# Optimization experiments

Hardware: AMD Instinct MI355X
Metric: run time of the kernel (lower is better)

## Reference

```python
import jax, jax.numpy as jnp
import numpy as np

B, S, E, H = 2, 2048, 1024, 16
D = E // H  # head_dim = 64


def setup_inputs() -> dict:
    key = jax.random.key(0)
    ks = jax.random.split(key, 5)
    return {
        "hidden_states": jax.random.normal(ks[0], (B, S, E), jnp.float32),
        "c_attn_w": jax.random.normal(ks[1], (E, 3 * E), jnp.float32) * 0.02,
        "c_attn_b": jnp.zeros((3 * E,), jnp.float32),
        "c_proj_w": jax.random.normal(ks[2], (E, E), jnp.float32) * 0.02,
        "c_proj_b": jnp.zeros((E,), jnp.float32),
    }


def reference(hidden_states, c_attn_w, c_attn_b, c_proj_w, c_proj_b):
    # Conv1D: x @ w + b -> qkv [B, S, 3E]
    qkv = hidden_states @ c_attn_w + c_attn_b
    q, k, v = jnp.split(qkv, 3, axis=-1)
    # [B, H, S, D]
    q = q.reshape(B, S, H, D).transpose(0, 2, 1, 3)
    k = k.reshape(B, S, H, D).transpose(0, 2, 1, 3)
    v = v.reshape(B, S, H, D).transpose(0, 2, 1, 3)
    # scores [B, H, S, S], scaled by sqrt(head_dim)
    scores = jnp.einsum("bhqd,bhkd->bhqk", q, k) / jnp.sqrt(jnp.asarray(D, q.dtype))
    causal = jnp.tril(jnp.ones((S, S), bool))  # [S, S]
    mask_value = jnp.finfo(scores.dtype).min
    scores = jnp.where(causal, scores, mask_value)
    attn = jax.nn.softmax(scores, axis=-1)
    # attn @ V -> [B, H, S, D] -> [B, S, E]
    out = jnp.einsum("bhqk,bhkd->bhqd", attn, v)
    out = out.transpose(0, 2, 1, 3).reshape(B, S, E)
    return out @ c_proj_w + c_proj_b
```

## Files before the change

kernel.cpp:

```cpp
#include <hip/hip_runtime.h>

using bf16 = __bf16;
typedef __bf16 bf16x8 __attribute__((ext_vector_type(8)));
typedef __bf16 bf16x4 __attribute__((ext_vector_type(4)));
typedef float  f32x4  __attribute__((ext_vector_type(4)));

#define MFMA16(a, b, c) __builtin_amdgcn_mfma_f32_16x16x32_bf16((a), (b), (c), 0, 0, 0)

static constexpr int S = 2048, E = 1024;
static constexpr float CSCALE = 0.18033688011112042f;

__device__ __forceinline__ void gld16(const bf16* g, bf16* l) {
    __builtin_amdgcn_global_load_lds((const __attribute__((address_space(1))) unsigned*)g,
                                     (__attribute__((address_space(3))) unsigned*)l, 16, 0, 0);
}

__global__ __launch_bounds__(256) void k_prep(const float* __restrict__ hs, const float* __restrict__ w0,
                                              const float* __restrict__ w1, bf16* __restrict__ A0,
                                              bf16* __restrict__ Wt0, bf16* __restrict__ Wt1) {
    __shared__ float tile[32][33];
    const int bx = blockIdx.x;
    if (bx < 4096) {
        int i = (bx * 256 + threadIdx.x) * 4;
        float4 v = *(const float4*)(hs + i);
        bf16x4 o = { (bf16)v.x, (bf16)v.y, (bf16)v.z, (bf16)v.w };
        *(bf16x4*)(A0 + i) = o;
        return;
    }
    const float* in;
    bf16* outp;
    int K, N, nb, kb;
    if (bx < 4096 + 3072) {
        int j = bx - 4096; in = w0; outp = Wt0; K = 1024; N = 3072; nb = j % 96; kb = j / 96;
    } else {
        int j = bx - 7168; in = w1; outp = Wt1; K = 1024; N = 1024; nb = j % 32; kb = j / 32;
    }
    const int bxx = nb * 32, byy = kb * 32;
    const int tx = threadIdx.x & 31, ty = threadIdx.x >> 5;
#pragma unroll
    for (int i = 0; i < 32; i += 8)
        tile[ty + i][tx] = in[(long)(byy + ty + i) * N + bxx + tx];
    __syncthreads();
#pragma unroll
    for (int i = 0; i < 32; i += 8)
        outp[(long)(bxx + ty + i) * K + byy + tx] = (bf16)tile[tx][ty + i];
}

__global__ __launch_bounds__(256) void k_gemm_qkv(const bf16* __restrict__ A, const bf16* __restrict__ Bt,
                                                  const float* __restrict__ bias, bf16* __restrict__ Qs,
                                                  bf16* __restrict__ Kf, bf16* __restrict__ Vf, int Kk) {
    const int bm = blockIdx.x * 128;
    const int bn = blockIdx.y * 128;
    const int tid = threadIdx.x;
    const int w = tid >> 6, lane = tid & 63;
    const int wm = (w >> 1) * 64, wn = (w & 1) * 64;
    const int col = lane & 15, quad = lane >> 4;

    __shared__ __align__(16) char smem[32768];
    bf16* sA = (bf16*)smem;
    bf16* sB = (bf16*)(smem + 16384);
    bf16* T  = (bf16*)smem;

    const bf16* pA[4]; const bf16* pB[4]; bf16* lA[4]; bf16* lB[4];
#pragma unroll
    for (int i = 0; i < 4; i++) {
        const int c = i * 256 + w * 64 + lane;
        const int r = c >> 3, sl = (c & 7) ^ (r & 7);
        pA[i] = A  + (long)(bm + r) * Kk + sl * 8;
        pB[i] = Bt + (long)(bn + r) * Kk + sl * 8;
        lA[i] = sA + i * 2048 + w * 512;
        lB[i] = sB + i * 2048 + w * 512;
    }

    f32x4 acc[4][4] = {};

    for (int k0 = 0; k0 < Kk; k0 += 64) {
        __syncthreads();
#pragma unroll
        for (int i = 0; i < 4; i++) gld16(pA[i] + k0, lA[i]);
#pragma unroll
        for (int i = 0; i < 4; i++) gld16(pB[i] + k0, lB[i]);
        __syncthreads();
#pragma unroll
        for (int h = 0; h < 2; h++) {
            bf16x8 af[4], bfr[4];
#pragma unroll
            for (int mt = 0; mt < 4; mt++) {
                const int row = wm + mt * 16 + col;
                af[mt] = *(const bf16x8*)(sA + row * 64 + (((h * 4 + quad) ^ (col & 7)) * 8));
            }
#pragma unroll
            for (int nt = 0; nt < 4; nt++) {
                const int row = wn + nt * 16 + col;
                bfr[nt] = *(const bf16x8*)(sB + row * 64 + (((h * 4 + quad) ^ (col & 7)) * 8));
            }
#pragma unroll
            for (int mt = 0; mt < 4; mt++)
#pragma unroll
                for (int nt = 0; nt < 4; nt++)
                    acc[mt][nt] = MFMA16(af[mt], bfr[nt], acc[mt][nt]);
        }
    }

    const int seg = bn >> 10;
    const int b = bm >> 11;
    const int kt0 = (bm & 2047) >> 6;

    if (seg == 0) {
#pragma unroll
        for (int mt = 0; mt < 4; mt++) {
            const int gr = bm + wm + mt * 16 + quad * 4;
#pragma unroll
            for (int nt = 0; nt < 4; nt++) {
                const int gc = bn + wn + nt * 16 + col;
                const float bv = bias[gc];
#pragma unroll
                for (int r = 0; r < 4; r++)
                    Qs[(long)(gr + r) * 1024 + gc] = (bf16)((acc[mt][nt][r] + bv) * CSCALE);
            }
        }
        return;
    }

    const int hl = w >> 1;
    if (seg == 1) {
        const int bh = b * 16 + (bn >> 6) - 16 + hl;
#pragma unroll 1
        for (int p = 0; p < 2; p++) {
            __syncthreads();
            if ((wm >> 6) == p) {
#pragma unroll
                for (int mt = 0; mt < 4; mt++) {
                    const int sl = mt * 16 + quad * 4;
#pragma unroll
                    for (int nt = 0; nt < 4; nt++) {
                        const int gcl = wn + nt * 16 + col;
                        const float bv = bias[bn + gcl];
#pragma unroll
                        for (int r = 0; r < 4; r++)
                            T[(sl + r) * 136 + gcl] = (bf16)(acc[mt][nt][r] + bv);
                    }
                }
            }
            __syncthreads();
            const int ktp = kt0 + p;
#pragma unroll
            for (int mi = 0; mi < 2; mi++) {
                const int mt = (w & 1) * 2 + mi;
#pragma unroll
                for (int half = 0; half < 2; half++) {
                    bf16x8 ch = *(const bf16x8*)(T + (mt * 16 + col) * 136 + hl * 64 + half * 32 + quad * 8);
                    const long chunk = ((long)(bh * 32 + ktp) * 8 + mt * 2 + half) * 64 + lane;
                    *(bf16x8*)(Kf + chunk * 8) = ch;
                }
            }
        }
    } else {
        const int bh = b * 16 + (bn >> 6) - 32 + hl;
#pragma unroll 1
        for (int p = 0; p < 2; p++) {
            __syncthreads();
            if ((wm >> 6) == p) {
#pragma unroll
                for (int mt = 0; mt < 4; mt++) {
                    const int sl = mt * 16 + quad * 4;
#pragma unroll
                    for (int nt = 0; nt < 4; nt++) {
                        const int gcl = wn + nt * 16 + col;
                        const float bv = bias[bn + gcl];
                        bf16x4 pk = { (bf16)(acc[mt][nt][0] + bv), (bf16)(acc[mt][nt][1] + bv),
                                      (bf16)(acc[mt][nt][2] + bv), (bf16)(acc[mt][nt][3] + bv) };
                        *(bf16x4*)(T + gcl * 72 + sl) = pk;
                    }
                }
            }
            __syncthreads();
            const int ktp = kt0 + p;
#pragma unroll
            for (int di = 0; di < 2; di++) {
                const int dt = (w & 1) * 2 + di;
#pragma unroll
                for (int ks = 0; ks < 2; ks++) {
                    bf16x8 ch = *(const bf16x8*)(T + (hl * 64 + dt * 16 + col) * 72 + ks * 32 + quad * 8);
                    const long chunk = ((long)(bh * 32 + ktp) * 8 + dt * 2 + ks) * 64 + lane;
                    *(bf16x8*)(Vf + chunk * 8) = ch;
                }
            }
        }
    }
}

__global__ __launch_bounds__(256) void k_gemm_bt64(const bf16* __restrict__ A, const bf16* __restrict__ Bt,
                                                    const float* __restrict__ bias, float* __restrict__ Cout,
                                                    int Mm, int Nn, int Kk) {
    const int bm = blockIdx.x * 64;
    const int bn = blockIdx.y * 128;
    const int tid = threadIdx.x;
    const int w = tid >> 6, lane = tid & 63;
    const int wm = (w >> 1) * 32, wn = (w & 1) * 64;
    const int col = lane & 15, quad = lane >> 4;

    __shared__ bf16 sA[64 * 64];
    __shared__ bf16 sB[128 * 64];

    const bf16* pA[2]; bf16* lA[2];
#pragma unroll
    for (int i = 0; i < 2; i++) {
        const int c = i * 256 + w * 64 + lane;
        const int r = c >> 3, sl = (c & 7) ^ (r & 7);
        pA[i] = A + (long)(bm + r) * Kk + sl * 8;
        lA[i] = sA + i * 2048 + w * 512;
    }
    const bf16* pB[4]; bf16* lB[4];
#pragma unroll
    for (int i = 0; i < 4; i++) {
        const int c = i * 256 + w * 64 + lane;
        const int r = c >> 3, sl = (c & 7) ^ (r & 7);
        pB[i] = Bt + (long)(bn + r) * Kk + sl * 8;
        lB[i] = sB + i * 2048 + w * 512;
    }

    f32x4 acc[2][4] = {};

    for (int k0 = 0; k0 < Kk; k0 += 64) {
        __syncthreads();
#pragma unroll
        for (int i = 0; i < 2; i++) gld16(pA[i] + k0, lA[i]);
#pragma unroll
        for (int i = 0; i < 4; i++) gld16(pB[i] + k0, lB[i]);
        __syncthreads();
#pragma unroll
        for (int h = 0; h < 2; h++) {
            bf16x8 af[2], bfr[4];
#pragma unroll
            for (int mt = 0; mt < 2; mt++) {
                const int row = wm + mt * 16 + col;
                af[mt] = *(const bf16x8*)(sA + row * 64 + (((h * 4 + quad) ^ (col & 7)) * 8));
            }
#pragma unroll
            for (int nt = 0; nt < 4; nt++) {
                const int row = wn + nt * 16 + col;
                bfr[nt] = *(const bf16x8*)(sB + row * 64 + (((h * 4 + quad) ^ (col & 7)) * 8));
            }
#pragma unroll
            for (int mt = 0; mt < 2; mt++)
#pragma unroll
                for (int nt = 0; nt < 4; nt++)
                    acc[mt][nt] = MFMA16(af[mt], bfr[nt], acc[mt][nt]);
        }
    }

#pragma unroll
    for (int mt = 0; mt < 2; mt++) {
        const int gr = bm + wm + mt * 16 + quad * 4;
#pragma unroll
        for (int nt = 0; nt < 4; nt++) {
            const int gc = bn + wn + nt * 16 + col;
            const float bv = bias[gc];
#pragma unroll
            for (int r = 0; r < 4; r++)
                Cout[(long)(gr + r) * Nn + gc] = acc[mt][nt][r] + bv;
        }
    }
}

__global__ __launch_bounds__(128) void k_attn(const bf16* __restrict__ Qs, const bf16* __restrict__ Kf,
                                              const bf16* __restrict__ Vf, bf16* __restrict__ out) {
    const int bh = blockIdx.x & 31;
    const int tp = blockIdx.x >> 5;
    const int b = bh >> 4, h = bh & 15;
    const int tid = threadIdx.x;
    const int w = tid >> 6, lane = tid & 63;
    const int col = lane & 15, quad = lane >> 4;

    __shared__ bf16 sP[2][32 * 72];
    __shared__ float M[2][64][36];
    bf16* pw = sP[w];

    const bf16* kfb = Kf + ((long)bh << 17) + lane * 8;
    const bf16* vfb = Vf + ((long)bh << 17) + lane * 8;

#pragma unroll 1
    for (int sel = 0; sel < 2; sel++) {
        const int t = sel ? 63 - tp : tp;
        const int q0 = t * 32;
        const int nkt = (t >> 1) + 1;
        const int kA = nkt >> 1;
        const int kbeg = w ? kA : 0;
        const int kend = w ? nkt : kA;

        bf16x8 bq[2][2];
#pragma unroll
        for (int qg = 0; qg < 2; qg++) {
            const bf16* qp = Qs + (long)(b * S + q0 + qg * 16 + col) * E + h * 64 + quad * 8;
            bq[qg][0] = *(const bf16x8*)(qp);
            bq[qg][1] = *(const bf16x8*)(qp + 32);
        }
        float m_[2] = { -1e30f, -1e30f }, l_[2] = { 0.f, 0.f };
        f32x4 o[2][4] = {};

#pragma unroll 1
        for (int kt = kbeg; kt < kend; kt++) {
            bf16x8 kfr[4][2], vfr[4][2];
#pragma unroll
            for (int mt = 0; mt < 4; mt++)
#pragma unroll
                for (int half = 0; half < 2; half++)
                    kfr[mt][half] = *(const bf16x8*)(kfb + ((long)(kt * 8 + mt * 2 + half) << 9));
#pragma unroll
            for (int dt = 0; dt < 4; dt++)
#pragma unroll
                for (int ks = 0; ks < 2; ks++)
                    vfr[dt][ks] = *(const bf16x8*)(vfb + ((long)(kt * 8 + dt * 2 + ks) << 9));

            f32x4 s[2][4];
#pragma unroll
            for (int mt = 0; mt < 4; mt++)
#pragma unroll
                for (int qg = 0; qg < 2; qg++) {
                    f32x4 z = {};
                    z = MFMA16(kfr[mt][0], bq[qg][0], z);
                    z = MFMA16(kfr[mt][1], bq[qg][1], z);
                    s[qg][mt] = z;
                }
            if (kt == nkt - 1) {
#pragma unroll
                for (int qg = 0; qg < 2; qg++) {
                    const int qrow = q0 + qg * 16 + col;
#pragma unroll
                    for (int mt = 0; mt < 4; mt++)
#pragma unroll
                        for (int r = 0; r < 4; r++)
                            if (kt * 64 + mt * 16 + quad * 4 + r > qrow) s[qg][mt][r] = -1e30f;
                }
            }
#pragma unroll
            for (int qg = 0; qg < 2; qg++) {
                float cm = -1e30f;
#pragma unroll
                for (int mt = 0; mt < 4; mt++)
#pragma unroll
                    for (int r = 0; r < 4; r++) cm = fmaxf(cm, s[qg][mt][r]);
                cm = fmaxf(cm, __shfl_xor(cm, 16));
                cm = fmaxf(cm, __shfl_xor(cm, 32));
                const float mnew = fmaxf(m_[qg], cm);
                const float alpha = __builtin_amdgcn_exp2f(m_[qg] - mnew);
                m_[qg] = mnew;
                float rs = 0.f;
#pragma unroll
                for (int mt = 0; mt < 4; mt++)
#pragma unroll
                    for (int r = 0; r < 4; r++) {
                        float pe = __builtin_amdgcn_exp2f(s[qg][mt][r] - mnew);
                        s[qg][mt][r] = pe;
                        rs += pe;
                    }
                l_[qg] = l_[qg] * alpha + rs;
#pragma unroll
                for (int dt = 0; dt < 4; dt++)
#pragma unroll
                    for (int r = 0; r < 4; r++) o[qg][dt][r] *= alpha;
#pragma unroll
                for (int mt = 0; mt < 4; mt++) {
                    bf16x4 pk = { (bf16)s[qg][mt][0], (bf16)s[qg][mt][1],
                                  (bf16)s[qg][mt][2], (bf16)s[qg][mt][3] };
                    *(bf16x4*)(pw + (qg * 16 + col) * 72 + mt * 16 + quad * 4) = pk;
                }
            }
#pragma unroll
            for (int ks = 0; ks < 2; ks++) {
                bf16x8 ap[2];
#pragma unroll
                for (int qg = 0; qg < 2; qg++)
                    ap[qg] = *(const bf16x8*)(pw + (qg * 16 + col) * 72 + ks * 32 + quad * 8);
#pragma unroll
                for (int dt = 0; dt < 4; dt++)
#pragma unroll
                    for (int qg = 0; qg < 2; qg++)
                        o[qg][dt] = MFMA16(vfr[dt][ks], ap[qg], o[qg][dt]);
            }
        }

#pragma unroll
        for (int qg = 0; qg < 2; qg++) {
            float lt = l_[qg];
            lt += __shfl_xor(lt, 16);
            lt += __shfl_xor(lt, 32);
            l_[qg] = lt;
        }

        if (w == 0) {
#pragma unroll
            for (int qg = 0; qg < 2; qg++) {
#pragma unroll
                for (int dt = 0; dt < 4; dt++)
                    *(f32x4*)&M[sel][lane][qg * 16 + dt * 4] = o[qg][dt];
                M[sel][lane][32 + qg * 2] = m_[qg];
                M[sel][lane][33 + qg * 2] = l_[qg];
            }
        }
        __syncthreads();
        if (w == 1) {
#pragma unroll
            for (int qg = 0; qg < 2; qg++) {
                const float m0 = M[sel][lane][32 + qg * 2];
                const float l0 = M[sel][lane][33 + qg * 2];
                const float mm = fmaxf(m0, m_[qg]);
                const float a0 = __builtin_amdgcn_exp2f(m0 - mm);
                const float a1 = __builtin_amdgcn_exp2f(m_[qg] - mm);
                const float li = 1.f / (l0 * a0 + l_[qg] * a1);
                bf16* op = out + (long)(b * S + q0 + qg * 16 + col) * E + h * 64 + quad * 4;
#pragma unroll
                for (int dt = 0; dt < 4; dt++) {
                    f32x4 o0 = *(const f32x4*)&M[sel][lane][qg * 16 + dt * 4];
                    bf16x4 ov;
#pragma unroll
                    for (int r = 0; r < 4; r++)
                        ov[r] = (bf16)((o0[r] * a0 + o[qg][dt][r] * a1) * li);
                    *(bf16x4*)(op + dt * 16) = ov;
                }
            }
        }
    }
}

extern "C" void kernel_launch(void* const* d_in, const int* in_sizes, int n_in,
                              void* d_out, int out_size, void* d_ws, size_t ws_size,
                              hipStream_t stream) {
    const float* hs = (const float*)d_in[0];
    const float* w0 = (const float*)d_in[1];
    const float* b0 = (const float*)d_in[2];
    const float* w1 = (const float*)d_in[3];
    const float* b1 = (const float*)d_in[4];
    float* outp = (float*)d_out;

    char* ws = (char*)d_ws;
    bf16* A0    = (bf16*)(ws);
    bf16* Wt0   = (bf16*)(ws + 8388608);
    bf16* Wt1   = (bf16*)(ws + 14680064);
    bf16* Qs    = (bf16*)(ws + 16777216);
    bf16* Kf    = (bf16*)(ws + 25165824);
    bf16* Vf    = (bf16*)(ws + 33554432);
    bf16* attnO = (bf16*)(ws + 41943040);

    k_prep<<<8192, 256, 0, stream>>>(hs, w0, w1, A0, Wt0, Wt1);
    k_gemm_qkv<<<dim3(32, 24), 256, 0, stream>>>(A0, Wt0, b0, Qs, Kf, Vf, 1024);
    k_attn<<<1024, 128, 0, stream>>>(Qs, Kf, Vf, attnO);
    k_gemm_bt64<<<dim3(64, 8), 256, 0, stream>>>(attnO, Wt1, b1, outp, 4096, 1024, 1024);
}
```

Measured before the change: 178.5 us.

## Split attention blocks to one query tile each and widen weight transpose tiles

The attention kernel used to pair a short and a long causal query tile in each block and loop over both. It now gives each block a single query tile, doubles the grid, and launches the longest tiles first so the scheduler can balance the load. The weight-transpose prep kernel now handles 64x32 tiles per block, which halves the number of transpose blocks and widens each bf16 store row. The trade-off is more, smaller attention blocks, so Q loads and block launch overhead are no longer amortized across a tile pair.

```diff
diff --git a/kernel.cpp b/kernel.cpp
--- a/kernel.cpp
+++ b/kernel.cpp
@@ -18,7 +18,7 @@
 __global__ __launch_bounds__(256) void k_prep(const float* __restrict__ hs, const float* __restrict__ w0,
                                               const float* __restrict__ w1, bf16* __restrict__ A0,
                                               bf16* __restrict__ Wt0, bf16* __restrict__ Wt1) {
-    __shared__ float tile[32][33];
+    __shared__ float tile[64][33];
     const int bx = blockIdx.x;
     if (bx < 4096) {
         int i = (bx * 256 + threadIdx.x) * 4;
@@ -30,20 +30,25 @@
     const float* in;
     bf16* outp;
     int K, N, nb, kb;
-    if (bx < 4096 + 3072) {
-        int j = bx - 4096; in = w0; outp = Wt0; K = 1024; N = 3072; nb = j % 96; kb = j / 96;
-    } else {
-        int j = bx - 7168; in = w1; outp = Wt1; K = 1024; N = 1024; nb = j % 32; kb = j / 32;
-    }
-    const int bxx = nb * 32, byy = kb * 32;
-    const int tx = threadIdx.x & 31, ty = threadIdx.x >> 5;
-#pragma unroll
-    for (int i = 0; i < 32; i += 8)
-        tile[ty + i][tx] = in[(long)(byy + ty + i) * N + bxx + tx];
+    const int j = bx - 4096;
+    if (j < 1536) { in = w0; outp = Wt0; K = 1024; N = 3072; nb = j % 96; kb = j / 96; }
+    else          { in = w1; outp = Wt1; K = 1024; N = 1024; nb = (j - 1536) % 32; kb = (j - 1536) / 32; }
+    const int bxx = nb * 32, byy = kb * 64;
+    {
+        const int r0 = threadIdx.x >> 5, c = threadIdx.x & 31;
+#pragma unroll
+        for (int i = 0; i < 8; i++)
+            tile[r0 + i * 8][c] = in[(long)(byy + r0 + i * 8) * N + bxx + c];
+    }
     __syncthreads();
-#pragma unroll
-    for (int i = 0; i < 32; i += 8)
-        outp[(long)(bxx + ty + i) * K + byy + tx] = (bf16)tile[tx][ty + i];
+    {
+        const int n0 = threadIdx.x >> 6, k = threadIdx.x & 63;
+#pragma unroll
+        for (int i = 0; i < 8; i++) {
+            const int n = n0 + i * 4;
+            outp[(long)(bxx + n) * K + byy + k] = (bf16)tile[k][n];
+        }
+    }
 }
 
 __global__ __launch_bounds__(256) void k_gemm_qkv(const bf16* __restrict__ A, const bf16* __restrict__ Bt,
@@ -267,158 +272,153 @@
 __global__ __launch_bounds__(128) void k_attn(const bf16* __restrict__ Qs, const bf16* __restrict__ Kf,
                                               const bf16* __restrict__ Vf, bf16* __restrict__ out) {
     const int bh = blockIdx.x & 31;
-    const int tp = blockIdx.x >> 5;
+    const int t = 63 - (blockIdx.x >> 5);
     const int b = bh >> 4, h = bh & 15;
     const int tid = threadIdx.x;
     const int w = tid >> 6, lane = tid & 63;
     const int col = lane & 15, quad = lane >> 4;
+    const int q0 = t * 32;
+    const int nkt = (t >> 1) + 1;
+    const int kA = nkt >> 1;
+    const int kbeg = w ? kA : 0;
+    const int kend = w ? nkt : kA;
 
     __shared__ bf16 sP[2][32 * 72];
-    __shared__ float M[2][64][36];
+    __shared__ float M[64][36];
     bf16* pw = sP[w];
 
     const bf16* kfb = Kf + ((long)bh << 17) + lane * 8;
     const bf16* vfb = Vf + ((long)bh << 17) + lane * 8;
 
+    bf16x8 bq[2][2];
+#pragma unroll
+    for (int qg = 0; qg < 2; qg++) {
+        const bf16* qp = Qs + (long)(b * S + q0 + qg * 16 + col) * E + h * 64 + quad * 8;
+        bq[qg][0] = *(const bf16x8*)(qp);
+        bq[qg][1] = *(const bf16x8*)(qp + 32);
+    }
+    float m_[2] = { -1e30f, -1e30f }, l_[2] = { 0.f, 0.f };
+    f32x4 o[2][4] = {};
+
 #pragma unroll 1
-    for (int sel = 0; sel < 2; sel++) {
-        const int t = sel ? 63 - tp : tp;
-        const int q0 = t * 32;
-        const int nkt = (t >> 1) + 1;
-        const int kA = nkt >> 1;
-        const int kbeg = w ? kA : 0;
-        const int kend = w ? nkt : kA;
-
-        bf16x8 bq[2][2];
+    for (int kt = kbeg; kt < kend; kt++) {
+        bf16x8 kfr[4][2], vfr[4][2];
+#pragma unroll
+        for (int mt = 0; mt < 4; mt++)
+#pragma unroll
+            for (int half = 0; half < 2; half++)
+                kfr[mt][half] = *(const bf16x8*)(kfb + ((long)(kt * 8 + mt * 2 + half) << 9));
+#pragma unroll
+        for (int dt = 0; dt < 4; dt++)
+#pragma unroll
+            for (int ks = 0; ks < 2; ks++)
+                vfr[dt][ks] = *(const bf16x8*)(vfb + ((long)(kt * 8 + dt * 2 + ks) << 9));
+
+        f32x4 s[2][4];
+#pragma unroll
+        for (int mt = 0; mt < 4; mt++)
+#pragma unroll
+            for (int qg = 0; qg < 2; qg++) {
+                f32x4 z = {};
+                z = MFMA16(kfr[mt][0], bq[qg][0], z);
+                z = MFMA16(kfr[mt][1], bq[qg][1], z);
+                s[qg][mt] = z;
+            }
+        if (kt == nkt - 1) {
+#pragma unroll
+            for (int qg = 0; qg < 2; qg++) {
+                const int qrow = q0 + qg * 16 + col;
+#pragma unroll
+                for (int mt = 0; mt < 4; mt++)
+#pragma unroll
+                    for (int r = 0; r < 4; r++)
+                        if (kt * 64 + mt * 16 + quad * 4 + r > qrow) s[qg][mt][r] = -1e30f;
+            }
+        }
 #pragma unroll
         for (int qg = 0; qg < 2; qg++) {
-            const bf16* qp = Qs + (long)(b * S + q0 + qg * 16 + col) * E + h * 64 + quad * 8;
-            bq[qg][0] = *(const bf16x8*)(qp);
-            bq[qg][1] = *(const bf16x8*)(qp + 32);
-        }
-        float m_[2] = { -1e30f, -1e30f }, l_[2] = { 0.f, 0.f };
-        f32x4 o[2][4] = {};
-
-#pragma unroll 1
-        for (int kt = kbeg; kt < kend; kt++) {
-            bf16x8 kfr[4][2], vfr[4][2];
+            float cm = -1e30f;
 #pragma unroll
             for (int mt = 0; mt < 4; mt++)
 #pragma unroll
-                for (int half = 0; half < 2; half++)
-                    kfr[mt][half] = *(const bf16x8*)(kfb + ((long)(kt * 8 + mt * 2 + half) << 9));
+                for (int r = 0; r < 4; r++) cm = fmaxf(cm, s[qg][mt][r]);
+            cm = fmaxf(cm, __shfl_xor(cm, 16));
+            cm = fmaxf(cm, __shfl_xor(cm, 32));
+            const float mnew = fmaxf(m_[qg], cm);
+            const float alpha = __builtin_amdgcn_exp2f(m_[qg] - mnew);
+            m_[qg] = mnew;
+            float rs = 0.f;
+#pragma unroll
+            for (int mt = 0; mt < 4; mt++)
+#pragma unroll
+                for (int r = 0; r < 4; r++) {
+                    float pe = __builtin_amdgcn_exp2f(s[qg][mt][r] - mnew);
+                    s[qg][mt][r] = pe;
+                    rs += pe;
+                }
+            l_[qg] = l_[qg] * alpha + rs;
 #pragma unroll
             for (int dt = 0; dt < 4; dt++)
 #pragma unroll
-                for (int ks = 0; ks < 2; ks++)
-                    vfr[dt][ks] = *(const bf16x8*)(vfb + ((long)(kt * 8 + dt * 2 + ks) << 9));
-
-            f32x4 s[2][4];
-#pragma unroll
-            for (int mt = 0; mt < 4; mt++)
-#pragma unroll
-                for (int qg = 0; qg < 2; qg++) {
-                    f32x4 z = {};
-                    z = MFMA16(kfr[mt][0], bq[qg][0], z);
-                    z = MFMA16(kfr[mt][1], bq[qg][1], z);
-                    s[qg][mt] = z;
-                }
-            if (kt == nkt - 1) {
-#pragma unroll
-                for (int qg = 0; qg < 2; qg++) {
-                    const int qrow = q0 + qg * 16 + col;
-#pragma unroll
-                    for (int mt = 0; mt < 4; mt++)
-#pragma unroll
-                        for (int r = 0; r < 4; r++)
-                            if (kt * 64 + mt * 16 + quad * 4 + r > qrow) s[qg][mt][r] = -1e30f;
-                }
-            }
-#pragma unroll
-            for (int qg = 0; qg < 2; qg++) {
-                float cm = -1e30f;
-#pragma unroll
-                for (int mt = 0; mt < 4; mt++)
-#pragma unroll
-                    for (int r = 0; r < 4; r++) cm = fmaxf(cm, s[qg][mt][r]);
-                cm = fmaxf(cm, __shfl_xor(cm, 16));
-                cm = fmaxf(cm, __shfl_xor(cm, 32));
-                const float mnew = fmaxf(m_[qg], cm);
-                const float alpha = __builtin_amdgcn_exp2f(m_[qg] - mnew);
-                m_[qg] = mnew;
-                float rs = 0.f;
-#pragma unroll
-                for (int mt = 0; mt < 4; mt++)
-#pragma unroll
-                    for (int r = 0; r < 4; r++) {
-                        float pe = __builtin_amdgcn_exp2f(s[qg][mt][r] - mnew);
-                        s[qg][mt][r] = pe;
-                        rs += pe;
-                    }
-                l_[qg] = l_[qg] * alpha + rs;
-#pragma unroll
-                for (int dt = 0; dt < 4; dt++)
-#pragma unroll
-                    for (int r = 0; r < 4; r++) o[qg][dt][r] *= alpha;
-#pragma unroll
-                for (int mt = 0; mt < 4; mt++) {
-                    bf16x4 pk = { (bf16)s[qg][mt][0], (bf16)s[qg][mt][1],
-                                  (bf16)s[qg][mt][2], (bf16)s[qg][mt][3] };
-                    *(bf16x4*)(pw + (qg * 16 + col) * 72 + mt * 16 + quad * 4) = pk;
-                }
-            }
-#pragma unroll
-            for (int ks = 0; ks < 2; ks++) {
-                bf16x8 ap[2];
+                for (int r = 0; r < 4; r++) o[qg][dt][r] *= alpha;
+#pragma unroll
+            for (int mt = 0; mt < 4; mt++) {
+                bf16x4 pk = { (bf16)s[qg][mt][0], (bf16)s[qg][mt][1],
+                              (bf16)s[qg][mt][2], (bf16)s[qg][mt][3] };
+                *(bf16x4*)(pw + (qg * 16 + col) * 72 + mt * 16 + quad * 4) = pk;
+            }
+        }
+#pragma unroll
+        for (int ks = 0; ks < 2; ks++) {
+            bf16x8 ap[2];
+#pragma unroll
+            for (int qg = 0; qg < 2; qg++)
+                ap[qg] = *(const bf16x8*)(pw + (qg * 16 + col) * 72 + ks * 32 + quad * 8);
+#pragma unroll
+            for (int dt = 0; dt < 4; dt++)
 #pragma unroll
                 for (int qg = 0; qg < 2; qg++)
-                    ap[qg] = *(const bf16x8*)(pw + (qg * 16 + col) * 72 + ks * 32 + quad * 8);
-#pragma unroll
-                for (int dt = 0; dt < 4; dt++)
-#pragma unroll
-                    for (int qg = 0; qg < 2; qg++)
-                        o[qg][dt] = MFMA16(vfr[dt][ks], ap[qg], o[qg][dt]);
-            }
-        }
-
+                    o[qg][dt] = MFMA16(vfr[dt][ks], ap[qg], o[qg][dt]);
+        }
+    }
+
+#pragma unroll
+    for (int qg = 0; qg < 2; qg++) {
+        float lt = l_[qg];
+        lt += __shfl_xor(lt, 16);
+        lt += __shfl_xor(lt, 32);
+        l_[qg] = lt;
+    }
+
+    if (w == 0) {
 #pragma unroll
         for (int qg = 0; qg < 2; qg++) {
-            float lt = l_[qg];
-            lt += __shfl_xor(lt, 16);
-            lt += __shfl_xor(lt, 32);
-            l_[qg] = lt;
-        }
-
-        if (w == 0) {
-#pragma unroll
-            for (int qg = 0; qg < 2; qg++) {
-#pragma unroll
-                for (int dt = 0; dt < 4; dt++)
-                    *(f32x4*)&M[sel][lane][qg * 16 + dt * 4] = o[qg][dt];
-                M[sel][lane][32 + qg * 2] = m_[qg];
-                M[sel][lane][33 + qg * 2] = l_[qg];
-            }
-        }
-        __syncthreads();
-        if (w == 1) {
-#pragma unroll
-            for (int qg = 0; qg < 2; qg++) {
-                const float m0 = M[sel][lane][32 + qg * 2];
-                const float l0 = M[sel][lane][33 + qg * 2];
-                const float mm = fmaxf(m0, m_[qg]);
-                const float a0 = __builtin_amdgcn_exp2f(m0 - mm);
-                const float a1 = __builtin_amdgcn_exp2f(m_[qg] - mm);
-                const float li = 1.f / (l0 * a0 + l_[qg] * a1);
-                bf16* op = out + (long)(b * S + q0 + qg * 16 + col) * E + h * 64 + quad * 4;
-#pragma unroll
-                for (int dt = 0; dt < 4; dt++) {
-                    f32x4 o0 = *(const f32x4*)&M[sel][lane][qg * 16 + dt * 4];
-                    bf16x4 ov;
-#pragma unroll
-                    for (int r = 0; r < 4; r++)
-                        ov[r] = (bf16)((o0[r] * a0 + o[qg][dt][r] * a1) * li);
-                    *(bf16x4*)(op + dt * 16) = ov;
-                }
+#pragma unroll
+            for (int dt = 0; dt < 4; dt++)
+                *(f32x4*)&M[lane][qg * 16 + dt * 4] = o[qg][dt];
+            M[lane][32 + qg * 2] = m_[qg];
+            M[lane][33 + qg * 2] = l_[qg];
+        }
+    }
+    __syncthreads();
+    if (w == 1) {
+#pragma unroll
+        for (int qg = 0; qg < 2; qg++) {
+            const float m0 = M[lane][32 + qg * 2];
+            const float l0 = M[lane][33 + qg * 2];
+            const float mm = fmaxf(m0, m_[qg]);
+            const float a0 = __builtin_amdgcn_exp2f(m0 - mm);
+            const float a1 = __builtin_amdgcn_exp2f(m_[qg] - mm);
+            const float li = 1.f / (l0 * a0 + l_[qg] * a1);
+            bf16* op = out + (long)(b * S + q0 + qg * 16 + col) * E + h * 64 + quad * 4;
+#pragma unroll
+            for (int dt = 0; dt < 4; dt++) {
+                f32x4 o0 = *(const f32x4*)&M[lane][qg * 16 + dt * 4];
+                bf16x4 ov;
+#pragma unroll
+                for (int r = 0; r < 4; r++)
+                    ov[r] = (bf16)((o0[r] * a0 + o[qg][dt][r] * a1) * li);
+                *(bf16x4*)(op + dt * 16) = ov;
             }
         }
     }
@@ -443,8 +443,8 @@
     bf16* Vf    = (bf16*)(ws + 33554432);
     bf16* attnO = (bf16*)(ws + 41943040);
 
-    k_prep<<<8192, 256, 0, stream>>>(hs, w0, w1, A0, Wt0, Wt1);
+    k_prep<<<6144, 256, 0, stream>>>(hs, w0, w1, A0, Wt0, Wt1);
     k_gemm_qkv<<<dim3(32, 24), 256, 0, stream>>>(A0, Wt0, b0, Qs, Kf, Vf, 1024);
-    k_attn<<<1024, 128, 0, stream>>>(Qs, Kf, Vf, attnO);
+    k_attn<<<2048, 128, 0, stream>>>(Qs, Kf, Vf, attnO);
     k_gemm_bt64<<<dim3(64, 8), 256, 0, stream>>>(attnO, Wt1, b1, outp, 4096, 1024, 1024);
 }
```

Measured after the change: 180.2 us. Within noise of the previous version (+0.9%).
